# Optimization experiments

Measured on AMD Instinct MI355X. Metric: run time of the kernel, lower is better.

## Reference

```python
import jax, jax.numpy as jnp
import numpy as np
from jax import lax

NUM_TAGS = 19
IN_DIM = 202
HID = 100
B, T = 256, 512


def setup_inputs() -> dict:
    key = jax.random.key(0)
    ks = jax.random.split(key, 16)
    u = lambda k, shape, s: jax.random.uniform(k, shape, jnp.float32, -s, s)
    sh = 1.0 / np.sqrt(HID)
    sl = 1.0 / np.sqrt(2 * HID)
    x = jax.random.normal(ks[0], (B, T, IN_DIM), jnp.float32)
    lengths = jax.random.randint(ks[1], (B,), 1, T + 1)
    raw_tags = jax.random.randint(ks[2], (B, T), 0, NUM_TAGS)
    y = jnp.where(jnp.arange(T)[None, :] < lengths[:, None], raw_tags, -1)
    return dict(
        x=x, y=y,
        w_ih_f=u(ks[3], (HID, IN_DIM), sh), w_hh_f=u(ks[4], (HID, HID), sh),
        b_ih_f=u(ks[5], (HID,), sh), b_hh_f=u(ks[6], (HID,), sh),
        w_ih_b=u(ks[7], (HID, IN_DIM), sh), w_hh_b=u(ks[8], (HID, HID), sh),
        b_ih_b=u(ks[9], (HID,), sh), b_hh_b=u(ks[10], (HID,), sh),
        w_lin=u(ks[11], (NUM_TAGS, 2 * HID), sl), b_lin=u(ks[12], (NUM_TAGS,), sl),
        start_trans=u(ks[13], (NUM_TAGS,), 0.1),
        end_trans=u(ks[14], (NUM_TAGS,), 0.1),
        trans=u(ks[15], (NUM_TAGS, NUM_TAGS), 0.1),
    )


def _rnn_dir(x, w_ih, w_hh, b_ih, b_hh, reverse):
    # torch nn.RNN (tanh) scans over axis 0 of x (batch_first=False semantics)
    def step(h, xt):
        h = jnp.tanh(xt @ w_ih.T + b_ih + h @ w_hh.T + b_hh)
        return h, h
    h0 = jnp.zeros((x.shape[1], w_hh.shape[0]), x.dtype)
    _, hs = lax.scan(step, h0, x, reverse=reverse)
    return hs  # (S, N, HID)


def _emissions(x, w_ih_f, w_hh_f, b_ih_f, b_hh_f, w_ih_b, w_hh_b, b_ih_b, b_hh_b, w_lin, b_lin):
    hf = _rnn_dir(x, w_ih_f, w_hh_f, b_ih_f, b_hh_f, False)
    hb = _rnn_dir(x, w_ih_b, w_hh_b, b_ih_b, b_hh_b, True)
    h = jnp.concatenate([hf, hb], axis=-1)  # (B, T, 200)
    return jax.nn.softmax(h @ w_lin.T + b_lin, axis=2)  # (B, T, 19)


def _crf_llh(em, tags, mask, start, end, trans):
    # emissions (B,T,K) batch_first -> transpose to (T,B,*) for the scans
    em_t = jnp.swapaxes(em, 0, 1)
    tg = jnp.where(jnp.swapaxes(mask, 0, 1), jnp.swapaxes(tags, 0, 1), 0)
    mk = jnp.swapaxes(mask, 0, 1)
    mf = mk.astype(em.dtype)
    # numerator: gold path score
    s0 = start[tg[0]] + jnp.take_along_axis(em_t[0], tg[0][:, None], 1)[:, 0]
    def num_step(carry, inp):
        s, prev = carry
        e, t, m, mb = inp
        emit = jnp.take_along_axis(e, t[:, None], 1)[:, 0]
        s = s + (trans[prev, t] + emit) * m
        prev = jnp.where(mb, t, prev)  # track tag at last valid position
        return (s, prev), None
    (num, last), _ = lax.scan(num_step, (s0, tg[0]), (em_t[1:], tg[1:], mf[1:], mk[1:]))
    num = num + end[last]
    # denominator: masked forward algorithm
    def z_step(s, inp):
        e, mb = inp
        nxt = jax.nn.logsumexp(s[:, :, None] + trans[None] + e[:, None, :], axis=1)
        return jnp.where(mb[:, None], nxt, s), None
    z, _ = lax.scan(z_step, start + em_t[0], (em_t[1:], mk[1:]))
    logz = jax.nn.logsumexp(z + end, axis=1)
    return num - logz  # (B,) log-likelihood per sequence


def _viterbi(em, mask, start, end, trans):
    em_t = jnp.swapaxes(em, 0, 1)
    mk = jnp.swapaxes(mask, 0, 1)
    def fstep(s, inp):
        e, mb = inp
        cand = s[:, :, None] + trans[None] + e[:, None, :]  # (B,K,K)
        nxt = jnp.where(mb[:, None], jnp.max(cand, axis=1), s)
        return nxt, jnp.argmax(cand, axis=1)
    score, hist = lax.scan(fstep, start + em_t[0], (em_t[1:], mk[1:]))  # hist (T-1,B,K)
    best_last = jnp.argmax(score + end, axis=1)  # tag at each sequence end
    def bstep(tag, inp):
        h, mb = inp
        prev = jnp.take_along_axis(h, tag[:, None], 1)[:, 0]
        tag = jnp.where(mb, prev, tag)
        return tag, tag
    _, tags_bt = lax.scan(bstep, best_last, (hist, mk[1:]), reverse=True)  # (T-1,B), position order
    tags = jnp.concatenate([tags_bt, best_last[None]], axis=0)  # (T,B)
    tags = jnp.swapaxes(tags, 0, 1)
    return jnp.where(mask, tags, -1)  # pad with -1 like the torch pad_sequence


def reference(x, y, w_ih_f, w_hh_f, b_ih_f, b_hh_f, w_ih_b, w_hh_b, b_ih_b, b_hh_b, w_lin, b_lin, start_trans, end_trans, trans):
    mask = y != -1
    em = _emissions(x, w_ih_f, w_hh_f, b_ih_f, b_hh_f, w_ih_b, w_hh_b, b_ih_b, b_hh_b, w_lin, b_lin)
    loss = -jnp.sum(_crf_llh(em, y, mask, start_trans, end_trans, trans))  # reduction='sum'
    label = _viterbi(em, mask, start_trans, end_trans, trans)
    return loss, label
```

## Files before the change

kernel.cpp:

```cpp
#include <hip/hip_runtime.h>
#include <hip/hip_bf16.h>

#define B_ 256
#define T_ 512
#define IN_ 202
#define HID_ 100
#define K_ 19

typedef __attribute__((ext_vector_type(8))) short short8v;
typedef __attribute__((ext_vector_type(4))) float f32x4;

__device__ __forceinline__ float rl_f(float v, int l) {
  return __int_as_float(__builtin_amdgcn_readlane(__float_as_int(v), l));
}

__global__ __launch_bounds__(256, 1) void k_wprep(
    const float* __restrict__ wf, const float* __restrict__ wb,
    unsigned short* __restrict__ w3) {
  int idx = blockIdx.x * 256 + threadIdx.x;
  if (idx >= 224 * 224) return;
  int c = idx / 224, k = idx - (idx / 224) * 224;
  float v = 0.f;
  if (k < IN_) {
    if (c < 100) v = wf[c * IN_ + k];
    else if (c < 200) v = wb[(c - 100) * IN_ + k];
  }
  unsigned u0 = __float_as_uint(v) & 0xffff0000u;
  float r1 = v - __uint_as_float(u0);
  unsigned u1 = __float_as_uint(r1) & 0xffff0000u;
  float r2 = r1 - __uint_as_float(u1);
  w3[idx] = (unsigned short)(u0 >> 16);
  w3[50176 + idx] = (unsigned short)(u1 >> 16);
  w3[100352 + idx] = (unsigned short)(__float_as_uint(r2) >> 16);
}

__global__ __launch_bounds__(256, 2) void k_ih(
    const float* __restrict__ x, const unsigned short* __restrict__ w3,
    const float* __restrict__ bif, const float* __restrict__ bhf,
    const float* __restrict__ bib, const float* __restrict__ bhb,
    float* __restrict__ pre) {
  __shared__ float xs[256 * 36];
  __shared__ float bsum[224];
  int tid = threadIdx.x;
  int wv = tid >> 6, l = tid & 63;
  long row0 = (long)blockIdx.x * 256;
  for (int u = tid; u < 224; u += 256) {
    float bv = 0.f;
    if (u < 100) bv = bif[u] + bhf[u];
    else if (u < 200) bv = bib[u - 100] + bhb[u - 100];
    bsum[u] = bv;
  }
  int lr = l & 15;
  int kq = l >> 4;
  for (int g = 0; g < 2; g++) {
    f32x4 acc[4][7];
#pragma unroll
    for (int m = 0; m < 4; m++)
#pragma unroll
      for (int n = 0; n < 7; n++) acc[m][n] = (f32x4){0.f, 0.f, 0.f, 0.f};
    for (int ck = 0; ck < 7; ck++) {
      int k0 = ck * 32;
      __syncthreads();
#pragma unroll
      for (int i = 0; i < 16; i++) {
        int u = tid + i * 256;
        int r = u >> 4, kp = u & 15;
        int gk = k0 + 2 * kp;
        float2 v = make_float2(0.f, 0.f);
        if (gk < IN_) v = *(const float2*)(x + (row0 + r) * IN_ + gk);
        *(float2*)(&xs[r * 36 + 2 * kp]) = v;
      }
      __syncthreads();
      short8v A0[4], A1[4], A2[4];
#pragma unroll
      for (int m = 0; m < 4; m++) {
        const float* ap = &xs[(wv * 64 + m * 16 + lr) * 36 + kq * 8];
        float4 fa = *(const float4*)(ap);
        float4 fb = *(const float4*)(ap + 4);
        float f[8] = {fa.x, fa.y, fa.z, fa.w, fb.x, fb.y, fb.z, fb.w};
#pragma unroll
        for (int j = 0; j < 8; j++) {
          unsigned u0 = __float_as_uint(f[j]) & 0xffff0000u;
          float r1 = f[j] - __uint_as_float(u0);
          unsigned u1 = __float_as_uint(r1) & 0xffff0000u;
          float r2 = r1 - __uint_as_float(u1);
          A0[m][j] = (short)(u0 >> 16);
          A1[m][j] = (short)(u1 >> 16);
          A2[m][j] = (short)(__float_as_uint(r2) >> 16);
        }
      }
#pragma unroll
      for (int n = 0; n < 7; n++) {
        int col = (g * 7 + n) * 16 + lr;
        const unsigned short* bp = w3 + (long)col * 224 + k0 + kq * 8;
        short8v B0 = *(const short8v*)(bp);
        short8v B1 = *(const short8v*)(bp + 50176);
        short8v B2 = *(const short8v*)(bp + 100352);
#pragma unroll
        for (int m = 0; m < 4; m++) {
          f32x4 c = acc[m][n];
          c = __builtin_amdgcn_mfma_f32_16x16x32_bf16(A0[m], B0, c, 0, 0, 0);
          c = __builtin_amdgcn_mfma_f32_16x16x32_bf16(A0[m], B1, c, 0, 0, 0);
          c = __builtin_amdgcn_mfma_f32_16x16x32_bf16(A1[m], B0, c, 0, 0, 0);
          c = __builtin_amdgcn_mfma_f32_16x16x32_bf16(A0[m], B2, c, 0, 0, 0);
          c = __builtin_amdgcn_mfma_f32_16x16x32_bf16(A2[m], B0, c, 0, 0, 0);
          c = __builtin_amdgcn_mfma_f32_16x16x32_bf16(A1[m], B1, c, 0, 0, 0);
          c = __builtin_amdgcn_mfma_f32_16x16x32_bf16(A1[m], B2, c, 0, 0, 0);
          c = __builtin_amdgcn_mfma_f32_16x16x32_bf16(A2[m], B1, c, 0, 0, 0);
          acc[m][n] = c;
        }
      }
    }
#pragma unroll
    for (int m = 0; m < 4; m++) {
      long rbase = row0 + wv * 64 + m * 16 + kq * 4;
#pragma unroll
      for (int n = 0; n < 7; n++) {
        int col = (g * 7 + n) * 16 + lr;
        if (col < 200) {
          float bv = bsum[col];
#pragma unroll
          for (int r = 0; r < 4; r++)
            pre[(rbase + r) * 200 + col] = acc[m][n][r] + bv;
        }
      }
    }
  }
}

template <int KO, int KN, bool OW>
__device__ __forceinline__ void rnn_loop(
    float* __restrict__ p, long step, int row, bool owns,
    const float* __restrict__ w, float (*hb)[104], float* __restrict__ ps) {
  float wr[KN];
#pragma unroll
  for (int i = 0; i < KN / 4; i++) {
    float4 w4 = *(const float4*)(w + row * HID_ + KO + 4 * i);
    wr[4 * i + 0] = w4.x; wr[4 * i + 1] = w4.y;
    wr[4 * i + 2] = w4.z; wr[4 * i + 3] = w4.w;
  }
  float a = 0.f;
  if (OW) a = p[row];
  for (int s = 0; s < B_; s++) {
    int cur = s & 1;
    float a_next = 0.f;
    if (OW && s < B_ - 1) a_next = p[step + row];
    float ac0 = OW ? a : 0.f, ac1 = 0.f, ac2 = 0.f, ac3 = 0.f;
#pragma unroll
    for (int i = 0; i < KN / 4; i++) {
      float4 h4 = *(const float4*)(&hb[cur][KO + 4 * i]);
      ac0 = fmaf(h4.x, wr[4 * i + 0], ac0);
      ac1 = fmaf(h4.y, wr[4 * i + 1], ac1);
      ac2 = fmaf(h4.z, wr[4 * i + 2], ac2);
      ac3 = fmaf(h4.w, wr[4 * i + 3], ac3);
    }
    float partial = (ac0 + ac1) + (ac2 + ac3);
    if (!OW && owns) ps[row] = partial;
    __syncthreads();
    if (OW) {
      float hnew = tanhf(partial + ps[row]);
      if (owns) {
        hb[cur ^ 1][row] = hnew;
        p[row] = hnew;
      }
    }
    p += step;
    a = a_next;
    __syncthreads();
  }
}

__global__ __launch_bounds__(256, 4) void k_rnn(
    float* __restrict__ pre,
    const float* __restrict__ whf, const float* __restrict__ whb) {
  __shared__ float hb[2][104];
  __shared__ float ps[104];
  int bid = blockIdx.x;
  int dir = bid >> 9;
  int t = bid & 511;
  const float* w = dir ? whb : whf;
  int tid = threadIdx.x;
  int wv = tid >> 6, lane = tid & 63;
  int grp = wv >> 1;
  int khalf = wv & 1;
  int row = grp ? (64 + (lane < 36 ? lane : 35)) : lane;
  bool owns = grp ? (lane < 36) : true;
  long step = dir ? -(long)(T_ * 200) : (long)(T_ * 200);
  float* p = pre + ((long)(dir ? (B_ - 1) : 0) * T_ + t) * 200 + dir * 100;
  if (tid < 104) hb[0][tid] = 0.f;
  __syncthreads();
  if (khalf == 0) rnn_loop<0, 52, true >(p, step, row, owns, w, hb, ps);
  else            rnn_loop<52, 48, false>(p, step, row, owns, w, hb, ps);
}

__global__ __launch_bounds__(256, 4) void k_lin(
    const float* __restrict__ h, const float* __restrict__ wlin,
    const float* __restrict__ blin, float* __restrict__ em) {
  int tid = threadIdx.x;
  long r0 = ((long)blockIdx.x * 256 + tid) * 2;
  const float* h0 = h + r0 * 200;
  float acc0[K_], acc1[K_];
#pragma unroll
  for (int c = 0; c < K_; c++) { float bb = blin[c]; acc0[c] = bb; acc1[c] = bb; }
  for (int kk = 0; kk < 50; kk++) {
    float4 a = *(const float4*)(h0 + 4 * kk);
    float4 b = *(const float4*)(h0 + 200 + 4 * kk);
#pragma unroll
    for (int c = 0; c < K_; c++) {
      float4 wv = *(const float4*)(wlin + c * 200 + 4 * kk);
      acc0[c] += a.x * wv.x + a.y * wv.y + a.z * wv.z + a.w * wv.w;
      acc1[c] += b.x * wv.x + b.y * wv.y + b.z * wv.z + b.w * wv.w;
    }
  }
  float mx0 = acc0[0], mx1 = acc1[0];
#pragma unroll
  for (int c = 1; c < K_; c++) { mx0 = fmaxf(mx0, acc0[c]); mx1 = fmaxf(mx1, acc1[c]); }
  float s0 = 0.f, s1 = 0.f;
#pragma unroll
  for (int c = 0; c < K_; c++) {
    acc0[c] = __expf(acc0[c] - mx0); s0 += acc0[c];
    acc1[c] = __expf(acc1[c] - mx1); s1 += acc1[c];
  }
  float i0 = 1.f / s0, i1 = 1.f / s1;
  float* e0 = em + r0 * K_;
#pragma unroll
  for (int c = 0; c < K_; c++) { e0[c] = acc0[c] * i0; e0[K_ + c] = acc1[c] * i1; }
}

__global__ __launch_bounds__(64, 1) void k_crf(
    const float* __restrict__ em, const int* __restrict__ y,
    const float* __restrict__ st_g, const float* __restrict__ en_g,
    const float* __restrict__ tr_g,
    float* __restrict__ part, int* __restrict__ cnt,
    float* __restrict__ out) {
  __shared__ __align__(16) float es[T_ * K_];
  __shared__ int ys[T_];
  __shared__ float trs[K_ * K_];
  __shared__ float st[K_], en[K_];
  __shared__ unsigned char hl[511 * K_ + 13];
  int b = blockIdx.x;
  int lane = threadIdx.x;
  const float4* eb4 = (const float4*)(em + (long)b * T_ * K_);
  for (int u = lane; u < T_ * K_ / 4; u += 64) ((float4*)es)[u] = eb4[u];
  for (int u = lane; u < T_; u += 64) ys[u] = y[b * T_ + u];
  for (int u = lane; u < K_ * K_; u += 64) trs[u] = tr_g[u];
  if (lane < K_) { st[lane] = st_g[lane]; en[lane] = en_g[lane]; }
  __syncthreads();
  int lmin = T_;
  for (int u = lane; u < T_; u += 64)
    if (ys[u] == -1 && u < lmin) lmin = u;
#pragma unroll
  for (int off = 32; off; off >>= 1) {
    int o = __shfl_xor(lmin, off, 64);
    lmin = lmin < o ? lmin : o;
  }
  int len = lmin;

  int jj = lane < K_ ? lane : K_ - 1;
  bool act = lane < K_;
  float E[K_], Tt[K_];
#pragma unroll
  for (int i = 0; i < K_; i++) {
    float tv = trs[i * K_ + jj];
    E[i] = __expf(tv);
    Tt[i] = tv;
  }
  float z = act ? st[jj] + es[jj] : -1e30f;
  float v = z;
  int prev = ys[0];
  float num = st[prev] + es[prev];
  float e = es[K_ + jj];
  for (int t = 1; t < len; t++) {
    int tn = t + 1 < T_ ? t + 1 : T_ - 1;
    float e_next = es[tn * K_ + jj];
    int yv = ys[t];
    float s = rl_f(z, 0);
    float pz = __expf(z - s);
    float acca = 0.f, accb = 0.f;
#pragma unroll
    for (int i = 0; i < 9; i++)  acca = fmaf(rl_f(pz, i), E[i], acca);
#pragma unroll
    for (int i = 9; i < K_; i++) accb = fmaf(rl_f(pz, i), E[i], accb);
    float nz = e + s + __logf(acca + accb);
    num += trs[prev * K_ + yv] + rl_f(e, yv);
    prev = yv;
    float b0 = -1e30f, b1 = -1e30f, b2 = -1e30f, b3 = -1e30f;
    int a0 = 0, a1 = 5, a2 = 10, a3 = 15;
#pragma unroll
    for (int i = 0; i < 5; i++)  { float c = rl_f(v, i) + Tt[i]; if (c > b0) { b0 = c; a0 = i; } }
#pragma unroll
    for (int i = 5; i < 10; i++) { float c = rl_f(v, i) + Tt[i]; if (c > b1) { b1 = c; a1 = i; } }
#pragma unroll
    for (int i = 10; i < 15; i++){ float c = rl_f(v, i) + Tt[i]; if (c > b2) { b2 = c; a2 = i; } }
#pragma unroll
    for (int i = 15; i < 19; i++){ float c = rl_f(v, i) + Tt[i]; if (c > b3) { b3 = c; a3 = i; } }
    if (b1 > b0) { b0 = b1; a0 = a1; }
    if (b2 > b0) { b0 = b2; a0 = a2; }
    if (b3 > b0) { b0 = b3; a0 = a3; }
    if (act) hl[(t - 1) * K_ + lane] = (unsigned char)a0;
    z = act ? nz : z;
    v = act ? b0 + e : v;
    e = e_next;
  }
  num += en[prev];
  float zf = act ? z + en[jj] : -1e30f;
  float m2 = zf;
#pragma unroll
  for (int off = 16; off; off >>= 1) m2 = fmaxf(m2, __shfl_xor(m2, off, 32));
  float sm = __expf(zf - m2);
#pragma unroll
  for (int off = 16; off; off >>= 1) sm += __shfl_xor(sm, off, 32);
  if (lane == 0) part[b] = m2 + __logf(sm) - num;
  float sc = act ? v + en[jj] : -1e30f;
  float bb = -1e30f; int aa = 0;
#pragma unroll
  for (int i = 0; i < K_; i++) { float c = rl_f(sc, i); if (c > bb) { bb = c; aa = i; } }
  float* ob = out + 1 + (long)b * T_;
  for (int u = lane; u < T_; u += 64)
    if (u >= len) ob[u] = -1.f;
  int tag = aa;
  if (lane == 0) ob[len - 1] = (float)tag;
  int vc = (act && len >= 2) ? (int)hl[(len - 2) * K_ + lane] : 0;
  for (int ti = len - 2; ti >= 0; ti--) {
    int vn = 0;
    if (ti > 0 && act) vn = (int)hl[(ti - 1) * K_ + lane];
    int ts = __builtin_amdgcn_readfirstlane(tag);
    tag = __builtin_amdgcn_readlane(vc, ts);
    if (lane == 0) ob[ti] = (float)tag;
    vc = vn;
  }
  int old = -1;
  if (lane == 0) { __threadfence(); old = atomicAdd(cnt, 1); }
  old = __shfl(old, 0, 64);
  if (old == B_ - 1) {
    __threadfence();
    float s = 0.f;
    for (int u = lane; u < B_; u += 64) s += part[u];
#pragma unroll
    for (int off = 32; off; off >>= 1) s += __shfl_xor(s, off, 64);
    if (lane == 0) out[0] = s;
  }
}

extern "C" void kernel_launch(void* const* d_in, const int* in_sizes, int n_in,
                              void* d_out, int out_size, void* d_ws, size_t ws_size,
                              hipStream_t stream) {
  const float* x      = (const float*)d_in[0];
  const int*   y      = (const int*)d_in[1];
  const float* w_ih_f = (const float*)d_in[2];
  const float* w_hh_f = (const float*)d_in[3];
  const float* b_ih_f = (const float*)d_in[4];
  const float* b_hh_f = (const float*)d_in[5];
  const float* w_ih_b = (const float*)d_in[6];
  const float* w_hh_b = (const float*)d_in[7];
  const float* b_ih_b = (const float*)d_in[8];
  const float* b_hh_b = (const float*)d_in[9];
  const float* w_lin  = (const float*)d_in[10];
  const float* b_lin  = (const float*)d_in[11];
  const float* st     = (const float*)d_in[12];
  const float* en     = (const float*)d_in[13];
  const float* trans  = (const float*)d_in[14];

  char* ws = (char*)d_ws;
  const size_t PRE_OFF  = 0;
  const size_t EM_OFF   = 104857600;
  const size_t PART_OFF = EM_OFF + 9961472;
  const size_t CNT_OFF  = PART_OFF + 1024;
  float* PRE  = (float*)(ws + PRE_OFF);
  float* EM   = (float*)(ws + EM_OFF);
  float* PART = (float*)(ws + PART_OFF);
  int*   CNT  = (int*)(ws + CNT_OFF);
  unsigned short* W3 = (unsigned short*)(ws + EM_OFF);
  float* out  = (float*)d_out;

  hipMemsetAsync((void*)CNT, 0, sizeof(int), stream);
  k_wprep<<<196, 256, 0, stream>>>(w_ih_f, w_ih_b, W3);
  k_ih<<<512, 256, 0, stream>>>(x, W3, b_ih_f, b_hh_f, b_ih_b, b_hh_b, PRE);
  k_rnn<<<1024, 256, 0, stream>>>(PRE, w_hh_f, w_hh_b);
  k_lin<<<256, 256, 0, stream>>>(PRE, w_lin, b_lin, EM);
  k_crf<<<256, 64, 0, stream>>>(EM, y, st, en, trans, PART, CNT, out);
}
```

Measured before the change: 703.9 us.

## Split CRF forward and Viterbi recursions across two wavefronts with LDS broadcast

The CRF kernel now runs with two wavefronts per block. One computes the log-partition forward recursion and the other runs the Viterbi max recursion and backtrace, so the two serial chains execute concurrently instead of interleaved in one wave. The per-step cross-lane broadcast moves from readlane chains to double-buffered LDS vectors read as float4. The gold-path numerator becomes a parallel strided sum with a wave reduction. The cost is LDS round-trip latency on every step and twice the threads per block.

New measurement: 652.3 us. 7.3% less time.

```diff
diff --git a/kernel.cpp b/kernel.cpp
--- a/kernel.cpp
+++ b/kernel.cpp
@@ -227,7 +227,7 @@
   for (int c = 0; c < K_; c++) { e0[c] = acc0[c] * i0; e0[K_ + c] = acc1[c] * i1; }
 }
 
-__global__ __launch_bounds__(64, 1) void k_crf(
+__global__ __launch_bounds__(128, 1) void k_crf(
     const float* __restrict__ em, const int* __restrict__ y,
     const float* __restrict__ st_g, const float* __restrict__ en_g,
     const float* __restrict__ tr_g,
@@ -238,13 +238,17 @@
   __shared__ float trs[K_ * K_];
   __shared__ float st[K_], en[K_];
   __shared__ unsigned char hl[511 * K_ + 13];
+  __shared__ __align__(16) float zbuf[2][20];
+  __shared__ __align__(16) float vbuf[2][20];
   int b = blockIdx.x;
-  int lane = threadIdx.x;
+  int tid = threadIdx.x;
+  int wv = tid >> 6, lane = tid & 63;
   const float4* eb4 = (const float4*)(em + (long)b * T_ * K_);
-  for (int u = lane; u < T_ * K_ / 4; u += 64) ((float4*)es)[u] = eb4[u];
-  for (int u = lane; u < T_; u += 64) ys[u] = y[b * T_ + u];
-  for (int u = lane; u < K_ * K_; u += 64) trs[u] = tr_g[u];
-  if (lane < K_) { st[lane] = st_g[lane]; en[lane] = en_g[lane]; }
+  for (int u = tid; u < T_ * K_ / 4; u += 128) ((float4*)es)[u] = eb4[u];
+  for (int u = tid; u < T_; u += 128) ys[u] = y[b * T_ + u];
+  for (int u = tid; u < K_ * K_; u += 128) trs[u] = tr_g[u];
+  if (tid < K_) { st[tid] = st_g[tid]; en[tid] = en_g[tid]; }
+  if (tid == 19) { zbuf[0][19] = -1e30f; zbuf[1][19] = -1e30f; vbuf[0][19] = -1e30f; vbuf[1][19] = -1e30f; }
   __syncthreads();
   int lmin = T_;
   for (int u = lane; u < T_; u += 64)
@@ -258,87 +262,145 @@
 
   int jj = lane < K_ ? lane : K_ - 1;
   bool act = lane < K_;
-  float E[K_], Tt[K_];
-#pragma unroll
-  for (int i = 0; i < K_; i++) {
-    float tv = trs[i * K_ + jj];
-    E[i] = __expf(tv);
-    Tt[i] = tv;
-  }
-  float z = act ? st[jj] + es[jj] : -1e30f;
-  float v = z;
-  int prev = ys[0];
-  float num = st[prev] + es[prev];
-  float e = es[K_ + jj];
-  for (int t = 1; t < len; t++) {
-    int tn = t + 1 < T_ ? t + 1 : T_ - 1;
-    float e_next = es[tn * K_ + jj];
-    int yv = ys[t];
-    float s = rl_f(z, 0);
-    float pz = __expf(z - s);
-    float acca = 0.f, accb = 0.f;
-#pragma unroll
-    for (int i = 0; i < 9; i++)  acca = fmaf(rl_f(pz, i), E[i], acca);
-#pragma unroll
-    for (int i = 9; i < K_; i++) accb = fmaf(rl_f(pz, i), E[i], accb);
-    float nz = e + s + __logf(acca + accb);
-    num += trs[prev * K_ + yv] + rl_f(e, yv);
-    prev = yv;
-    float b0 = -1e30f, b1 = -1e30f, b2 = -1e30f, b3 = -1e30f;
-    int a0 = 0, a1 = 5, a2 = 10, a3 = 15;
-#pragma unroll
-    for (int i = 0; i < 5; i++)  { float c = rl_f(v, i) + Tt[i]; if (c > b0) { b0 = c; a0 = i; } }
-#pragma unroll
-    for (int i = 5; i < 10; i++) { float c = rl_f(v, i) + Tt[i]; if (c > b1) { b1 = c; a1 = i; } }
-#pragma unroll
-    for (int i = 10; i < 15; i++){ float c = rl_f(v, i) + Tt[i]; if (c > b2) { b2 = c; a2 = i; } }
-#pragma unroll
-    for (int i = 15; i < 19; i++){ float c = rl_f(v, i) + Tt[i]; if (c > b3) { b3 = c; a3 = i; } }
-    if (b1 > b0) { b0 = b1; a0 = a1; }
-    if (b2 > b0) { b0 = b2; a0 = a2; }
-    if (b3 > b0) { b0 = b3; a0 = a3; }
-    if (act) hl[(t - 1) * K_ + lane] = (unsigned char)a0;
-    z = act ? nz : z;
-    v = act ? b0 + e : v;
-    e = e_next;
-  }
-  num += en[prev];
-  float zf = act ? z + en[jj] : -1e30f;
-  float m2 = zf;
-#pragma unroll
-  for (int off = 16; off; off >>= 1) m2 = fmaxf(m2, __shfl_xor(m2, off, 32));
-  float sm = __expf(zf - m2);
-#pragma unroll
-  for (int off = 16; off; off >>= 1) sm += __shfl_xor(sm, off, 32);
-  if (lane == 0) part[b] = m2 + __logf(sm) - num;
-  float sc = act ? v + en[jj] : -1e30f;
-  float bb = -1e30f; int aa = 0;
-#pragma unroll
-  for (int i = 0; i < K_; i++) { float c = rl_f(sc, i); if (c > bb) { bb = c; aa = i; } }
-  float* ob = out + 1 + (long)b * T_;
-  for (int u = lane; u < T_; u += 64)
-    if (u >= len) ob[u] = -1.f;
-  int tag = aa;
-  if (lane == 0) ob[len - 1] = (float)tag;
-  int vc = (act && len >= 2) ? (int)hl[(len - 2) * K_ + lane] : 0;
-  for (int ti = len - 2; ti >= 0; ti--) {
-    int vn = 0;
-    if (ti > 0 && act) vn = (int)hl[(ti - 1) * K_ + lane];
-    int ts = __builtin_amdgcn_readfirstlane(tag);
-    tag = __builtin_amdgcn_readlane(vc, ts);
-    if (lane == 0) ob[ti] = (float)tag;
-    vc = vn;
-  }
-  int old = -1;
-  if (lane == 0) { __threadfence(); old = atomicAdd(cnt, 1); }
-  old = __shfl(old, 0, 64);
-  if (old == B_ - 1) {
-    __threadfence();
-    float s = 0.f;
-    for (int u = lane; u < B_; u += 64) s += part[u];
-#pragma unroll
-    for (int off = 32; off; off >>= 1) s += __shfl_xor(s, off, 64);
-    if (lane == 0) out[0] = s;
+  float enr[20];
+#pragma unroll
+  for (int q = 0; q < 5; q++) {
+    float4 e4 = (q < 4) ? *(const float4*)(&en[4 * q])
+                        : make_float4(en[16], en[17], en[18], -1e30f);
+    enr[4 * q] = e4.x; enr[4 * q + 1] = e4.y; enr[4 * q + 2] = e4.z; enr[4 * q + 3] = e4.w;
+  }
+
+  if (wv == 0) {
+    float gacc = 0.f;
+    for (int t = 1 + lane; t < len; t += 64)
+      gacc += trs[ys[t - 1] * K_ + ys[t]] + es[t * K_ + ys[t]];
+#pragma unroll
+    for (int off = 32; off; off >>= 1) gacc += __shfl_xor(gacc, off, 64);
+    int y0 = ys[0], ylast = ys[len - 1];
+    float num = st[y0] + es[y0] + gacc + en[ylast];
+    float E[K_];
+#pragma unroll
+    for (int i = 0; i < K_; i++) E[i] = __expf(trs[i * K_ + jj]);
+    if (act) zbuf[0][lane] = st[jj] + es[jj];
+    asm volatile("s_waitcnt lgkmcnt(0)" ::: "memory");
+    for (int t = 1; t < len; t++) {
+      int cur = (t - 1) & 1;
+      float zr[20];
+#pragma unroll
+      for (int q = 0; q < 5; q++) {
+        float4 z4 = *(const float4*)(&zbuf[cur][4 * q]);
+        zr[4 * q] = z4.x; zr[4 * q + 1] = z4.y; zr[4 * q + 2] = z4.z; zr[4 * q + 3] = z4.w;
+      }
+      float e = es[t * K_ + jj];
+      float s = zr[0];
+      float p0 = 1.f;
+      float a0 = p0 * E[0], a1 = 0.f, a2 = 0.f, a3 = 0.f;
+#pragma unroll
+      for (int i = 1; i < K_; i++) {
+        float pz = __expf(zr[i] - s);
+        if ((i & 3) == 1)      a1 = fmaf(pz, E[i], a1);
+        else if ((i & 3) == 2) a2 = fmaf(pz, E[i], a2);
+        else if ((i & 3) == 3) a3 = fmaf(pz, E[i], a3);
+        else                   a0 = fmaf(pz, E[i], a0);
+      }
+      float nz = e + s + __logf((a0 + a1) + (a2 + a3));
+      if (act) zbuf[cur ^ 1][lane] = nz;
+      asm volatile("s_waitcnt lgkmcnt(0)" ::: "memory");
+    }
+    {
+      int cur = (len - 1) & 1;
+      float zr[20];
+#pragma unroll
+      for (int q = 0; q < 5; q++) {
+        float4 z4 = *(const float4*)(&zbuf[cur][4 * q]);
+        zr[4 * q] = z4.x; zr[4 * q + 1] = z4.y; zr[4 * q + 2] = z4.z; zr[4 * q + 3] = z4.w;
+      }
+      float zf[K_];
+#pragma unroll
+      for (int i = 0; i < K_; i++) zf[i] = zr[i] + enr[i];
+      float m2 = zf[0];
+#pragma unroll
+      for (int i = 1; i < K_; i++) m2 = fmaxf(m2, zf[i]);
+      float sm = 0.f;
+#pragma unroll
+      for (int i = 0; i < K_; i++) sm += __expf(zf[i] - m2);
+      if (lane == 0) part[b] = m2 + __logf(sm) - num;
+    }
+    int old = -1;
+    if (lane == 0) { __threadfence(); old = atomicAdd(cnt, 1); }
+    old = __shfl(old, 0, 64);
+    if (old == B_ - 1) {
+      __threadfence();
+      float s = 0.f;
+      for (int u = lane; u < B_; u += 64) s += part[u];
+#pragma unroll
+      for (int off = 32; off; off >>= 1) s += __shfl_xor(s, off, 64);
+      if (lane == 0) out[0] = s;
+    }
+  } else {
+    float Tt[K_];
+#pragma unroll
+    for (int i = 0; i < K_; i++) Tt[i] = trs[i * K_ + jj];
+    if (act) vbuf[0][lane] = st[jj] + es[jj];
+    asm volatile("s_waitcnt lgkmcnt(0)" ::: "memory");
+    for (int t = 1; t < len; t++) {
+      int cur = (t - 1) & 1;
+      float vr[20];
+#pragma unroll
+      for (int q = 0; q < 5; q++) {
+        float4 v4 = *(const float4*)(&vbuf[cur][4 * q]);
+        vr[4 * q] = v4.x; vr[4 * q + 1] = v4.y; vr[4 * q + 2] = v4.z; vr[4 * q + 3] = v4.w;
+      }
+      float e = es[t * K_ + jj];
+      float b0 = -1e30f, b1 = -1e30f, b2 = -1e30f, b3 = -1e30f;
+      int a0 = 0, a1 = 5, a2 = 10, a3 = 15;
+#pragma unroll
+      for (int i = 0; i < 5; i++)  { float c = vr[i] + Tt[i]; if (c > b0) { b0 = c; a0 = i; } }
+#pragma unroll
+      for (int i = 5; i < 10; i++) { float c = vr[i] + Tt[i]; if (c > b1) { b1 = c; a1 = i; } }
+#pragma unroll
+      for (int i = 10; i < 15; i++){ float c = vr[i] + Tt[i]; if (c > b2) { b2 = c; a2 = i; } }
+#pragma unroll
+      for (int i = 15; i < 19; i++){ float c = vr[i] + Tt[i]; if (c > b3) { b3 = c; a3 = i; } }
+      if (b1 > b0) { b0 = b1; a0 = a1; }
+      if (b2 > b0) { b0 = b2; a0 = a2; }
+      if (b3 > b0) { b0 = b3; a0 = a3; }
+      if (act) {
+        hl[(t - 1) * K_ + lane] = (unsigned char)a0;
+        vbuf[cur ^ 1][lane] = b0 + e;
+      }
+      asm volatile("s_waitcnt lgkmcnt(0)" ::: "memory");
+    }
+    int aa;
+    {
+      int cur = (len - 1) & 1;
+      float vr[20];
+#pragma unroll
+      for (int q = 0; q < 5; q++) {
+        float4 v4 = *(const float4*)(&vbuf[cur][4 * q]);
+        vr[4 * q] = v4.x; vr[4 * q + 1] = v4.y; vr[4 * q + 2] = v4.z; vr[4 * q + 3] = v4.w;
+      }
+      float bb = vr[0] + enr[0]; aa = 0;
+#pragma unroll
+      for (int i = 1; i < K_; i++) {
+        float c = vr[i] + enr[i];
+        if (c > bb) { bb = c; aa = i; }
+      }
+    }
+    float* ob = out + 1 + (long)b * T_;
+    for (int u = lane; u < T_; u += 64)
+      if (u >= len) ob[u] = -1.f;
+    int tag = aa;
+    if (lane == 0) ob[len - 1] = (float)tag;
+    int vc = (act && len >= 2) ? (int)hl[(len - 2) * K_ + lane] : 0;
+    for (int ti = len - 2; ti >= 0; ti--) {
+      int vn = 0;
+      if (ti > 0 && act) vn = (int)hl[(ti - 1) * K_ + lane];
+      int ts = __builtin_amdgcn_readfirstlane(tag);
+      tag = __builtin_amdgcn_readlane(vc, ts);
+      if (lane == 0) ob[ti] = (float)tag;
+      vc = vn;
+    }
   }
 }
 
@@ -378,5 +440,5 @@
   k_ih<<<512, 256, 0, stream>>>(x, W3, b_ih_f, b_hh_f, b_ih_b, b_hh_b, PRE);
   k_rnn<<<1024, 256, 0, stream>>>(PRE, w_hh_f, w_hh_b);
   k_lin<<<256, 256, 0, stream>>>(PRE, w_lin, b_lin, EM);
-  k_crf<<<256, 64, 0, stream>>>(EM, y, st, en, trans, PART, CNT, out);
-}
+  k_crf<<<256, 128, 0, stream>>>(EM, y, st, en, trans, PART, CNT, out);
+}
```
